# Optimization experiments

Hardware: AMD Instinct MI355X
Metric: run time of the kernel (lower is better)

## Reference

```python
import jax, jax.numpy as jnp
import numpy as np

B, T, H = 32, 2048, 1024

def setup_inputs() -> dict:
    key = jax.random.key(0)
    ks = jax.random.split(key, 9)
    s = 1.0 / np.sqrt(H)
    return {
        "encoder_outputs": jax.random.normal(ks[0], (B, T, H), jnp.float32),
        "decoder_output": jax.random.normal(ks[1], (1, B, H), jnp.float32),
        "Wk": jax.random.uniform(ks[2], (H, H), jnp.float32, -s, s),
        "bk": jax.random.uniform(ks[3], (H,), jnp.float32, -s, s),
        "Wq": jax.random.uniform(ks[4], (H, H), jnp.float32, -s, s),
        "bq": jax.random.uniform(ks[5], (H,), jnp.float32, -s, s),
        "Wout": jax.random.uniform(ks[6], (H,), jnp.float32, -s, s),
        "bout": jax.random.uniform(ks[7], (), jnp.float32, -s, s),
        "inputs": jax.random.randint(ks[8], (B, T), 0, 32000, jnp.int32),  # unused, as in original
    }

def reference(encoder_outputs, decoder_output, Wk, bk, Wq, bq, Wout, bout, inputs):
    # decoder_output: [1, B, H] -> [B, 1, H]
    dec = jnp.swapaxes(decoder_output, 0, 1)
    k = encoder_outputs @ Wk.T + bk          # [B, T, H]
    q = dec @ Wq.T + bq                      # [B, 1, H]
    score = jnp.tanh(k + q) @ Wout + bout    # [B, T]  (linear_out squeezed)
    attn = jax.nn.softmax(score, axis=-1)    # [B, T]
    context = jnp.einsum('bt,bth->bh', attn, encoder_outputs)  # [B, H]
    return context[:, None, :]               # [B, 1, H]
```

## Files before the change

### kernel.cpp

```cpp
#include <hip/hip_runtime.h>
#include <cmath>
#include <stdint.h>

#define B_ 32
#define T_ 2048
#define H_ 1024

typedef __attribute__((ext_vector_type(8))) __bf16 bf16x8;
typedef __attribute__((ext_vector_type(4))) float f32x4;

__device__ inline void async_copy16(const void* g, void* l) {
    __builtin_amdgcn_global_load_lds((const __attribute__((address_space(1))) uint32_t*)g,
                                     (__attribute__((address_space(3))) uint32_t*)l, 16, 0, 0);
}

__device__ inline float fast_tanh(float x) {
    float e = __expf(2.f * x);
    return 1.f - 2.f / (e + 1.f);
}

__global__ __launch_bounds__(256) void zero_kernel(float* __restrict__ p, int n) {
    int i = blockIdx.x * 256 + threadIdx.x;
    if (i < n) p[i] = 0.f;
}

__global__ __launch_bounds__(256) void convert_kernel(const float* __restrict__ in,
                                                      __bf16* __restrict__ out) {
    size_t i = (size_t)(blockIdx.x * 256 + threadIdx.x) * 8;
    const float4* p = (const float4*)(in + i);
    float4 v0 = p[0], v1 = p[1];
    bf16x8 o;
    o[0] = (__bf16)v0.x; o[1] = (__bf16)v0.y; o[2] = (__bf16)v0.z; o[3] = (__bf16)v0.w;
    o[4] = (__bf16)v1.x; o[5] = (__bf16)v1.y; o[6] = (__bf16)v1.z; o[7] = (__bf16)v1.w;
    *(bf16x8*)(out + i) = o;
}

__global__ __launch_bounds__(256) void q_kernel(const float* __restrict__ dec,
                                                const float* __restrict__ Wq,
                                                const float* __restrict__ bq,
                                                const float* __restrict__ bk,
                                                float* __restrict__ kq) {
    int b = blockIdx.x;
    int hc = blockIdx.y;
    __shared__ float ds[H_];
    for (int i = threadIdx.x; i < H_; i += 256) ds[i] = dec[b * H_ + i];
    __syncthreads();
    int h = hc * 256 + threadIdx.x;
    const float4* w = (const float4*)(Wq + (size_t)h * H_);
    float acc = 0.f;
#pragma unroll 8
    for (int j = 0; j < H_ / 4; j++) {
        float4 v = w[j];
        acc += v.x * ds[4 * j] + v.y * ds[4 * j + 1] + v.z * ds[4 * j + 2] + v.w * ds[4 * j + 3];
    }
    kq[b * H_ + h] = acc + bq[h] + bk[h];
}

__global__ __launch_bounds__(256) void score_mfma(const __bf16* __restrict__ encb,
                                                  const __bf16* __restrict__ Wkb,
                                                  const float* __restrict__ kq,
                                                  const float* __restrict__ Wout,
                                                  float* __restrict__ sp) {
    __shared__ __align__(16) __bf16 As[1024 * 8];
    __shared__ __align__(16) __bf16 Bs[1024 * 8];

    const int bid = blockIdx.x;
    const int xcd = bid & 7;
    const int g = (bid >> 3) & 7;
    const int mt = (bid >> 6) * 8 + xcd;
    const int h0 = g * 128;
    const int m0 = mt * 128;
    const int b = m0 >> 11;
    const int tid = threadIdx.x;
    const int lane = tid & 63;
    const int w = tid >> 6;
    const int wm = w & 1, wn = w >> 1;
    const int q4 = lane >> 4, l15 = lane & 15;

    int kgs[4], rows[4];
    const __bf16 *gA[4], *gB[4];
    __bf16 *lA[4], *lB[4];
#pragma unroll
    for (int r = 0; r < 4; r++) {
        int S = w * 256 + r * 64 + lane;
        kgs[r] = S >> 7;
        rows[r] = S & 127;
        gA[r] = encb + (size_t)(m0 + rows[r]) * H_ + kgs[r] * 8;
        gB[r] = Wkb + (size_t)(h0 + rows[r]) * H_ + kgs[r] * 8;
        lA[r] = As + (size_t)(w * 256 + r * 64) * 8;
        lB[r] = Bs + (size_t)(w * 256 + r * 64) * 8;
    }

    f32x4 acc[4][4];
#pragma unroll
    for (int i = 0; i < 4; i++)
#pragma unroll
        for (int j = 0; j < 4; j++) acc[i][j] = (f32x4){0.f, 0.f, 0.f, 0.f};

    for (int k0 = 0; k0 < H_; k0 += 64) {
        __syncthreads();
#pragma unroll
        for (int r = 0; r < 4; r++) async_copy16(gA[r] + k0, lA[r]);
#pragma unroll
        for (int r = 0; r < 4; r++) async_copy16(gB[r] + k0, lB[r]);
        __syncthreads();

#pragma unroll
        for (int kb = 0; kb < 2; kb++) {
            bf16x8 a[4], bb[4];
#pragma unroll
            for (int mf = 0; mf < 4; mf++)
                a[mf] = *(const bf16x8*)(As + (size_t)(((kb * 4 + q4) * 128) + wm * 64 + mf * 16 + l15) * 8);
#pragma unroll
            for (int nf = 0; nf < 4; nf++)
                bb[nf] = *(const bf16x8*)(Bs + (size_t)(((kb * 4 + q4) * 128) + wn * 64 + nf * 16 + l15) * 8);
#pragma unroll
            for (int mf = 0; mf < 4; mf++)
#pragma unroll
                for (int nf = 0; nf < 4; nf++)
                    acc[mf][nf] = __builtin_amdgcn_mfma_f32_16x16x32_bf16(a[mf], bb[nf], acc[mf][nf], 0, 0, 0);
        }
    }

    float wv[4], kqv[4];
#pragma unroll
    for (int nf = 0; nf < 4; nf++) {
        int h = h0 + wn * 64 + nf * 16 + l15;
        wv[nf] = Wout[h];
        kqv[nf] = kq[b * H_ + h];
    }
    const size_t slice = (size_t)(g * 2 + wn) * (B_ * T_);
#pragma unroll
    for (int mf = 0; mf < 4; mf++) {
#pragma unroll
        for (int r = 0; r < 4; r++) {
            float s = 0.f;
#pragma unroll
            for (int nf = 0; nf < 4; nf++)
                s += wv[nf] * fast_tanh(acc[mf][nf][r] + kqv[nf]);
#pragma unroll
            for (int m = 1; m < 16; m <<= 1) s += __shfl_xor(s, m, 64);
            if (l15 == 0)
                sp[slice + m0 + wm * 64 + mf * 16 + q4 * 4 + r] = s;
        }
    }
}

__global__ __launch_bounds__(256) void softmax_kernel(const float* __restrict__ sp,
                                                      float* __restrict__ attn) {
    int b = blockIdx.x, tid = threadIdx.x;
    __shared__ float red[8];
    float v[8];
    float mx = -1e30f;
#pragma unroll
    for (int i = 0; i < 8; i++) {
        int t = tid + i * 256;
        float s = 0.f;
#pragma unroll
        for (int sl = 0; sl < 16; sl++) s += sp[(size_t)sl * (B_ * T_) + b * T_ + t];
        v[i] = s;
        mx = fmaxf(mx, s);
    }
#pragma unroll
    for (int m = 32; m >= 1; m >>= 1) mx = fmaxf(mx, __shfl_xor(mx, m, 64));
    if ((tid & 63) == 0) red[tid >> 6] = mx;
    __syncthreads();
    mx = fmaxf(fmaxf(red[0], red[1]), fmaxf(red[2], red[3]));
    float sum = 0.f;
#pragma unroll
    for (int i = 0; i < 8; i++) {
        v[i] = __expf(v[i] - mx);
        sum += v[i];
    }
#pragma unroll
    for (int m = 32; m >= 1; m >>= 1) sum += __shfl_xor(sum, m, 64);
    if ((tid & 63) == 0) red[4 + (tid >> 6)] = sum;
    __syncthreads();
    sum = red[4] + red[5] + red[6] + red[7];
    float inv = 1.f / sum;
#pragma unroll
    for (int i = 0; i < 8; i++) attn[b * T_ + tid + i * 256] = v[i] * inv;
}

__global__ __launch_bounds__(256) void context_part(const float* __restrict__ enc,
                                                    const float* __restrict__ attn,
                                                    float* __restrict__ cpart) {
    int ts = blockIdx.x, b = blockIdx.y;
    const float* e = enc + (size_t)b * T_ * H_ + (size_t)ts * 64 * H_ + threadIdx.x * 4;
    const float* a = attn + b * T_ + ts * 64;
    float4 acc = {0.f, 0.f, 0.f, 0.f};
#pragma unroll 4
    for (int t = 0; t < 64; t++) {
        float av = a[t];
        float4 v = *(const float4*)(e + (size_t)t * H_);
        acc.x += av * v.x; acc.y += av * v.y; acc.z += av * v.z; acc.w += av * v.w;
    }
    *(float4*)(cpart + ((size_t)b * 32 + ts) * H_ + threadIdx.x * 4) = acc;
}

__global__ __launch_bounds__(256) void context_reduce(const float* __restrict__ cpart,
                                                      float* __restrict__ out) {
    int hc = blockIdx.x, b = blockIdx.y;
    int h = hc * 256 + threadIdx.x;
    float s = 0.f;
#pragma unroll
    for (int ts = 0; ts < 32; ts++) s += cpart[((size_t)b * 32 + ts) * H_ + h];
    out[b * H_ + h] = s;
}

#define BK 32
#define ASTR 68
#define BSTR 132
__global__ __launch_bounds__(256) void score_fp32(const float* __restrict__ enc,
                                                  const float* __restrict__ Wk,
                                                  const float* __restrict__ kq,
                                                  const float* __restrict__ Wout,
                                                  float* __restrict__ score) {
    __shared__ __align__(16) float As2[BK * ASTR];
    __shared__ __align__(16) float Bs2[BK * BSTR];
    __shared__ float wout_s[128];
    __shared__ float kq_s[128];
    const int m0 = blockIdx.x * 64;
    const int h0 = blockIdx.y * 128;
    const int b = m0 >> 11;
    const int tid = threadIdx.x;
    const int tx = tid & 15;
    const int ty = tid >> 4;
    if (tid < 128) {
        wout_s[tid] = Wout[h0 + tid];
        kq_s[tid] = kq[b * H_ + h0 + tid];
    }
    float acc[4][8];
#pragma unroll
    for (int i = 0; i < 4; i++)
#pragma unroll
        for (int j = 0; j < 8; j++) acc[i][j] = 0.f;
    for (int k0 = 0; k0 < H_; k0 += BK) {
        __syncthreads();
#pragma unroll
        for (int r = 0; r < 2; r++) {
            int li = tid + r * 256;
            int tok = li >> 3, kg = li & 7;
            float4 v = *(const float4*)(enc + (size_t)(m0 + tok) * H_ + k0 + kg * 4);
            As2[(kg * 4 + 0) * ASTR + tok] = v.x;
            As2[(kg * 4 + 1) * ASTR + tok] = v.y;
            As2[(kg * 4 + 2) * ASTR + tok] = v.z;
            As2[(kg * 4 + 3) * ASTR + tok] = v.w;
        }
#pragma unroll
        for (int r = 0; r < 4; r++) {
            int li = tid + r * 256;
            int h = li >> 3, kg = li & 7;
            float4 v = *(const float4*)(Wk + (size_t)(h0 + h) * H_ + k0 + kg * 4);
            Bs2[(kg * 4 + 0) * BSTR + h] = v.x;
            Bs2[(kg * 4 + 1) * BSTR + h] = v.y;
            Bs2[(kg * 4 + 2) * BSTR + h] = v.z;
            Bs2[(kg * 4 + 3) * BSTR + h] = v.w;
        }
        __syncthreads();
#pragma unroll
        for (int kk = 0; kk < BK; kk++) {
            float4 a4 = *(const float4*)&As2[kk * ASTR + ty * 4];
            float4 b4a = *(const float4*)&Bs2[kk * BSTR + tx * 4];
            float4 b4b = *(const float4*)&Bs2[kk * BSTR + 64 + tx * 4];
            float av[4] = {a4.x, a4.y, a4.z, a4.w};
            float bv[8] = {b4a.x, b4a.y, b4a.z, b4a.w, b4b.x, b4b.y, b4b.z, b4b.w};
#pragma unroll
            for (int i = 0; i < 4; i++)
#pragma unroll
                for (int j = 0; j < 8; j++) acc[i][j] += av[i] * bv[j];
        }
    }
    float wv[8], kqv[8];
#pragma unroll
    for (int j = 0; j < 8; j++) {
        int hl = (j < 4) ? (tx * 4 + j) : (64 + tx * 4 + (j - 4));
        wv[j] = wout_s[hl];
        kqv[j] = kq_s[hl];
    }
#pragma unroll
    for (int i = 0; i < 4; i++) {
        float s = 0.f;
#pragma unroll
        for (int j = 0; j < 8; j++) s += wv[j] * tanhf(acc[i][j] + kqv[j]);
#pragma unroll
        for (int m = 1; m < 16; m <<= 1) s += __shfl_xor(s, m, 64);
        if (tx == 0) atomicAdd(&score[m0 + ty * 4 + i], s);
    }
}

__global__ __launch_bounds__(256) void softmax_inplace(float* __restrict__ score) {
    int b = blockIdx.x, tid = threadIdx.x;
    float* s = score + b * T_;
    __shared__ float red[8];
    float v[8];
    float mx = -1e30f;
#pragma unroll
    for (int i = 0; i < 8; i++) {
        v[i] = s[tid + i * 256];
        mx = fmaxf(mx, v[i]);
    }
#pragma unroll
    for (int m = 32; m >= 1; m >>= 1) mx = fmaxf(mx, __shfl_xor(mx, m, 64));
    if ((tid & 63) == 0) red[tid >> 6] = mx;
    __syncthreads();
    mx = fmaxf(fmaxf(red[0], red[1]), fmaxf(red[2], red[3]));
    float sum = 0.f;
#pragma unroll
    for (int i = 0; i < 8; i++) {
        v[i] = __expf(v[i] - mx);
        sum += v[i];
    }
#pragma unroll
    for (int m = 32; m >= 1; m >>= 1) sum += __shfl_xor(sum, m, 64);
    if ((tid & 63) == 0) red[4 + (tid >> 6)] = sum;
    __syncthreads();
    sum = red[4] + red[5] + red[6] + red[7];
    float inv = 1.f / sum;
#pragma unroll
    for (int i = 0; i < 8; i++) s[tid + i * 256] = v[i] * inv;
}

extern "C" void kernel_launch(void* const* d_in, const int* in_sizes, int n_in,
                              void* d_out, int out_size, void* d_ws, size_t ws_size,
                              hipStream_t stream) {
    const float* enc = (const float*)d_in[0];
    const float* dec = (const float*)d_in[1];
    const float* Wk = (const float*)d_in[2];
    const float* bk = (const float*)d_in[3];
    const float* Wq = (const float*)d_in[4];
    const float* bq = (const float*)d_in[5];
    const float* Wout = (const float*)d_in[6];
    float* out = (float*)d_out;

    const size_t encb_bytes = (size_t)B_ * T_ * H_ * 2;
    const size_t wkb_bytes = (size_t)H_ * H_ * 2;
    const size_t kq_bytes = (size_t)B_ * H_ * 4;
    const size_t attn_bytes = (size_t)B_ * T_ * 4;
    const size_t sp_bytes = (size_t)16 * B_ * T_ * 4;
    const size_t cpart_bytes = (size_t)B_ * 32 * H_ * 4;
    const size_t shared_bytes = sp_bytes > cpart_bytes ? sp_bytes : cpart_bytes;
    const size_t need = encb_bytes + wkb_bytes + kq_bytes + attn_bytes + shared_bytes;

    if (ws_size >= need) {
        char* p = (char*)d_ws;
        __bf16* encb = (__bf16*)p;            p += encb_bytes;
        __bf16* Wkb = (__bf16*)p;             p += wkb_bytes;
        float* kq = (float*)p;                p += kq_bytes;
        float* attn = (float*)p;              p += attn_bytes;
        float* sp = (float*)p;
        float* cpart = (float*)p;

        convert_kernel<<<(B_ * T_ * H_) / 2048, 256, 0, stream>>>(enc, encb);
        convert_kernel<<<(H_ * H_) / 2048, 256, 0, stream>>>(Wk, Wkb);
        q_kernel<<<dim3(B_, 4), 256, 0, stream>>>(dec, Wq, bq, bk, kq);
        score_mfma<<<4096, 256, 0, stream>>>(encb, Wkb, kq, Wout, sp);
        softmax_kernel<<<B_, 256, 0, stream>>>(sp, attn);
        context_part<<<dim3(32, B_), 256, 0, stream>>>(enc, attn, cpart);
        context_reduce<<<dim3(4, B_), 256, 0, stream>>>(cpart, out);
    } else {
        float* kq = (float*)d_ws;
        float* score = kq + B_ * H_;
        float* cpart = score + B_ * T_;
        q_kernel<<<dim3(B_, 4), 256, 0, stream>>>(dec, Wq, bq, bk, kq);
        zero_kernel<<<(B_ * T_ + 255) / 256, 256, 0, stream>>>(score, B_ * T_);
        score_fp32<<<dim3(1024, 8), 256, 0, stream>>>(enc, Wk, kq, Wout, score);
        softmax_inplace<<<B_, 256, 0, stream>>>(score);
        context_part<<<dim3(32, B_), 256, 0, stream>>>(enc, score, cpart);
        context_reduce<<<dim3(4, B_), 256, 0, stream>>>(cpart, out);
    }
}
```

Baseline: 772.6 us.

## Loop all H column tiles per block with double-buffered LDS and in-block score reduction

```diff
diff --git a/kernel.cpp b/kernel.cpp
--- a/kernel.cpp
+++ b/kernel.cpp
@@ -61,15 +61,11 @@
                                                   const float* __restrict__ kq,
                                                   const float* __restrict__ Wout,
                                                   float* __restrict__ sp) {
-    __shared__ __align__(16) __bf16 As[1024 * 8];
-    __shared__ __align__(16) __bf16 Bs[1024 * 8];
-
-    const int bid = blockIdx.x;
-    const int xcd = bid & 7;
-    const int g = (bid >> 3) & 7;
-    const int mt = (bid >> 6) * 8 + xcd;
-    const int h0 = g * 128;
-    const int m0 = mt * 128;
+    __shared__ __align__(16) __bf16 As[2][512 * 8];
+    __shared__ __align__(16) __bf16 Bs[2][512 * 8];
+    __shared__ float red[256];
+
+    const int m0 = blockIdx.x * 128;
     const int b = m0 >> 11;
     const int tid = threadIdx.x;
     const int lane = tid & 63;
@@ -77,18 +73,15 @@
     const int wm = w & 1, wn = w >> 1;
     const int q4 = lane >> 4, l15 = lane & 15;
 
-    int kgs[4], rows[4];
-    const __bf16 *gA[4], *gB[4];
-    __bf16 *lA[4], *lB[4];
-#pragma unroll
-    for (int r = 0; r < 4; r++) {
-        int S = w * 256 + r * 64 + lane;
-        kgs[r] = S >> 7;
-        rows[r] = S & 127;
-        gA[r] = encb + (size_t)(m0 + rows[r]) * H_ + kgs[r] * 8;
-        gB[r] = Wkb + (size_t)(h0 + rows[r]) * H_ + kgs[r] * 8;
-        lA[r] = As + (size_t)(w * 256 + r * 64) * 8;
-        lB[r] = Bs + (size_t)(w * 256 + r * 64) * 8;
+    const __bf16 *baseA[2], *baseB[2];
+    uint32_t ldsOff[2];
+#pragma unroll
+    for (int r = 0; r < 2; r++) {
+        int S = r * 256 + tid;
+        int kg = S >> 7, row = S & 127;
+        baseA[r] = encb + (size_t)(m0 + row) * H_ + kg * 8;
+        baseB[r] = Wkb + (size_t)row * H_ + kg * 8;
+        ldsOff[r] = (uint32_t)(r * 256 + w * 64) * 8;
     }
 
     f32x4 acc[4][4];
@@ -97,69 +90,101 @@
 #pragma unroll
         for (int j = 0; j < 4; j++) acc[i][j] = (f32x4){0.f, 0.f, 0.f, 0.f};
 
-    for (int k0 = 0; k0 < H_; k0 += 64) {
+    float srow[4][4];
+#pragma unroll
+    for (int i = 0; i < 4; i++)
+#pragma unroll
+        for (int r = 0; r < 4; r++) srow[i][r] = 0.f;
+
+    float wv[4] = {0.f, 0.f, 0.f, 0.f}, kqv[4] = {0.f, 0.f, 0.f, 0.f};
+
+#pragma unroll
+    for (int r = 0; r < 2; r++) {
+        async_copy16(baseA[r], &As[0][ldsOff[r]]);
+        async_copy16(baseB[r], &Bs[0][ldsOff[r]]);
+    }
+
+    for (int it = 0; it < 256; ++it) {
+        const int cur = it & 1;
+        const int g = it >> 5;
+
         __syncthreads();
-#pragma unroll
-        for (int r = 0; r < 4; r++) async_copy16(gA[r] + k0, lA[r]);
-#pragma unroll
-        for (int r = 0; r < 4; r++) async_copy16(gB[r] + k0, lB[r]);
-        __syncthreads();
-
-#pragma unroll
-        for (int kb = 0; kb < 2; kb++) {
-            bf16x8 a[4], bb[4];
+
+        if (it < 255) {
+            const int it1 = it + 1;
+            const size_t offA = (size_t)((it1 & 31) << 5);
+            const size_t offB = (size_t)(it1 >> 5) * (size_t)(128 * H_) + (size_t)((it1 & 31) << 5);
+#pragma unroll
+            for (int r = 0; r < 2; r++) {
+                async_copy16(baseA[r] + offA, &As[cur ^ 1][ldsOff[r]]);
+                async_copy16(baseB[r] + offB, &Bs[cur ^ 1][ldsOff[r]]);
+            }
+        }
+
+        if ((it & 31) == 0) {
+#pragma unroll
+            for (int nf = 0; nf < 4; nf++) {
+                int h = g * 128 + wn * 64 + nf * 16 + l15;
+                wv[nf] = Wout[h];
+                kqv[nf] = kq[b * H_ + h];
+            }
+        }
+
+        bf16x8 a[4], bb[4];
+#pragma unroll
+        for (int mf = 0; mf < 4; mf++)
+            a[mf] = *(const bf16x8*)(&As[cur][(size_t)(q4 * 128 + wm * 64 + mf * 16 + l15) * 8]);
+#pragma unroll
+        for (int nf = 0; nf < 4; nf++)
+            bb[nf] = *(const bf16x8*)(&Bs[cur][(size_t)(q4 * 128 + wn * 64 + nf * 16 + l15) * 8]);
+#pragma unroll
+        for (int mf = 0; mf < 4; mf++)
+#pragma unroll
+            for (int nf = 0; nf < 4; nf++)
+                acc[mf][nf] = __builtin_amdgcn_mfma_f32_16x16x32_bf16(a[mf], bb[nf], acc[mf][nf], 0, 0, 0);
+
+        if ((it & 31) == 31) {
 #pragma unroll
             for (int mf = 0; mf < 4; mf++)
-                a[mf] = *(const bf16x8*)(As + (size_t)(((kb * 4 + q4) * 128) + wm * 64 + mf * 16 + l15) * 8);
-#pragma unroll
-            for (int nf = 0; nf < 4; nf++)
-                bb[nf] = *(const bf16x8*)(Bs + (size_t)(((kb * 4 + q4) * 128) + wn * 64 + nf * 16 + l15) * 8);
-#pragma unroll
-            for (int mf = 0; mf < 4; mf++)
-#pragma unroll
-                for (int nf = 0; nf < 4; nf++)
-                    acc[mf][nf] = __builtin_amdgcn_mfma_f32_16x16x32_bf16(a[mf], bb[nf], acc[mf][nf], 0, 0, 0);
-        }
-    }
-
-    float wv[4], kqv[4];
-#pragma unroll
-    for (int nf = 0; nf < 4; nf++) {
-        int h = h0 + wn * 64 + nf * 16 + l15;
-        wv[nf] = Wout[h];
-        kqv[nf] = kq[b * H_ + h];
-    }
-    const size_t slice = (size_t)(g * 2 + wn) * (B_ * T_);
-#pragma unroll
-    for (int mf = 0; mf < 4; mf++) {
+#pragma unroll
+                for (int r = 0; r < 4; r++) {
+                    float s = 0.f;
+#pragma unroll
+                    for (int nf = 0; nf < 4; nf++)
+                        s += wv[nf] * fast_tanh(acc[mf][nf][r] + kqv[nf]);
+                    srow[mf][r] += s;
+                }
+#pragma unroll
+            for (int i = 0; i < 4; i++)
+#pragma unroll
+                for (int j = 0; j < 4; j++) acc[i][j] = (f32x4){0.f, 0.f, 0.f, 0.f};
+        }
+    }
+
+#pragma unroll
+    for (int mf = 0; mf < 4; mf++)
 #pragma unroll
         for (int r = 0; r < 4; r++) {
-            float s = 0.f;
-#pragma unroll
-            for (int nf = 0; nf < 4; nf++)
-                s += wv[nf] * fast_tanh(acc[mf][nf][r] + kqv[nf]);
+            float s = srow[mf][r];
 #pragma unroll
             for (int m = 1; m < 16; m <<= 1) s += __shfl_xor(s, m, 64);
-            if (l15 == 0)
-                sp[slice + m0 + wm * 64 + mf * 16 + q4 * 4 + r] = s;
-        }
-    }
+            if (l15 == 0) red[wn * 128 + wm * 64 + mf * 16 + q4 * 4 + r] = s;
+        }
+    __syncthreads();
+    if (tid < 128) sp[m0 + tid] = red[tid] + red[128 + tid];
 }
 
 __global__ __launch_bounds__(256) void softmax_kernel(const float* __restrict__ sp,
                                                       float* __restrict__ attn) {
     int b = blockIdx.x, tid = threadIdx.x;
+    const float* s = sp + b * T_;
     __shared__ float red[8];
     float v[8];
     float mx = -1e30f;
 #pragma unroll
     for (int i = 0; i < 8; i++) {
-        int t = tid + i * 256;
-        float s = 0.f;
-#pragma unroll
-        for (int sl = 0; sl < 16; sl++) s += sp[(size_t)sl * (B_ * T_) + b * T_ + t];
-        v[i] = s;
-        mx = fmaxf(mx, s);
+        v[i] = s[tid + i * 256];
+        mx = fmaxf(mx, v[i]);
     }
 #pragma unroll
     for (int m = 32; m >= 1; m >>= 1) mx = fmaxf(mx, __shfl_xor(mx, m, 64));
@@ -337,7 +362,7 @@
     const size_t wkb_bytes = (size_t)H_ * H_ * 2;
     const size_t kq_bytes = (size_t)B_ * H_ * 4;
     const size_t attn_bytes = (size_t)B_ * T_ * 4;
-    const size_t sp_bytes = (size_t)16 * B_ * T_ * 4;
+    const size_t sp_bytes = (size_t)B_ * T_ * 4;
     const size_t cpart_bytes = (size_t)B_ * 32 * H_ * 4;
     const size_t shared_bytes = sp_bytes > cpart_bytes ? sp_bytes : cpart_bytes;
     const size_t need = encb_bytes + wkb_bytes + kq_bytes + attn_bytes + shared_bytes;
@@ -354,7 +379,7 @@
         convert_kernel<<<(B_ * T_ * H_) / 2048, 256, 0, stream>>>(enc, encb);
         convert_kernel<<<(H_ * H_) / 2048, 256, 0, stream>>>(Wk, Wkb);
         q_kernel<<<dim3(B_, 4), 256, 0, stream>>>(dec, Wq, bq, bk, kq);
-        score_mfma<<<4096, 256, 0, stream>>>(encb, Wkb, kq, Wout, sp);
+        score_mfma<<<512, 256, 0, stream>>>(encb, Wkb, kq, Wout, sp);
         softmax_kernel<<<B_, 256, 0, stream>>>(sp, attn);
         context_part<<<dim3(32, B_), 256, 0, stream>>>(enc, attn, cpart);
         context_reduce<<<dim3(4, B_), 256, 0, stream>>>(cpart, out);
```

New measurement: 823.1 us. +6.5%, slower.
